# Kernel optimization log

Measured on AMD Instinct MI355X. Metric: run time of the kernel, lower is better.

Reference implementation:

```python
import jax, jax.numpy as jnp
import numpy as np

B, H, W, C = 8, 64, 64, 64
CFG = C // 8  # filters for f and g


def setup_inputs() -> dict:
    key = jax.random.key(0)
    kx, kf, kg, kh = jax.random.split(key, 4)
    x = jax.random.normal(kx, (B, H, W, C), dtype=jnp.float32)
    # 1x1 conv kernels, Keras layout (kh, kw, in_ch, out_ch); glorot-scale init
    kernel_f = jax.random.normal(kf, (1, 1, C, CFG), dtype=jnp.float32) * (2.0 / (C + CFG)) ** 0.5
    kernel_g = jax.random.normal(kg, (1, 1, C, CFG), dtype=jnp.float32) * (2.0 / (C + CFG)) ** 0.5
    kernel_h = jax.random.normal(kh, (1, 1, C, C), dtype=jnp.float32) * (2.0 / (C + C)) ** 0.5
    gamma = jnp.zeros((1,), dtype=jnp.float32)
    return {"x": x, "kernel_f": kernel_f, "kernel_g": kernel_g, "kernel_h": kernel_h, "gamma": gamma}


def reference(x, kernel_f, kernel_g, kernel_h, gamma):
    b, h, w, c = x.shape
    n = h * w
    xf = x.reshape(b, n, c)  # hw_flatten; 1x1 conv == per-pixel matmul
    f = jnp.einsum('bnc,cd->bnd', xf, kernel_f[0, 0])  # [B, N, C//8]
    g = jnp.einsum('bnc,cd->bnd', xf, kernel_g[0, 0])  # [B, N, C//8]
    hh = jnp.einsum('bnc,cd->bnd', xf, kernel_h[0, 0])  # [B, N, C]
    s = jnp.einsum('bqd,bkd->bqk', g, f)  # unscaled attention scores [B, N, N]
    beta = jax.nn.softmax(s, axis=-1)
    o = jnp.einsum('bqk,bkc->bqc', beta, hh).reshape(b, h, w, c)
    return gamma * o + x
```

## Files before the change

kernel.cpp:

```cpp
#include <hip/hip_runtime.h>
#include <hip/hip_bf16.h>


#define NPIX 4096
#define CH 64

typedef float f32x4 __attribute__((ext_vector_type(4)));
typedef short s16x8 __attribute__((ext_vector_type(8)));
typedef unsigned int u32x4 __attribute__((ext_vector_type(4)));
typedef unsigned short u16;
typedef unsigned int u32;
typedef unsigned long long u64;

__device__ __forceinline__ u16 f32_to_bf16(float f) {
  u32 u = __builtin_bit_cast(u32, f);
  u += 0x7fffu + ((u >> 16) & 1u);
  return (u16)(u >> 16);
}
__device__ __forceinline__ u32 pack_bf16(float lo, float hi) {
  return (u32)f32_to_bf16(lo) | ((u32)f32_to_bf16(hi) << 16);
}
__device__ __forceinline__ u32 cvt_pk_bf16(float lo, float hi) {
  u32 d;
  asm("v_cvt_pk_bf16_f32 %0, %1, %2" : "=v"(d) : "v"(lo), "v"(hi));
  return d;
}
__device__ __forceinline__ void gload_lds16(const void* g, void* l) {
  __builtin_amdgcn_global_load_lds(
      (const __attribute__((address_space(1))) unsigned int*)g,
      (__attribute__((address_space(3))) unsigned int*)l, 16, 0, 0);
}

__global__ __launch_bounds__(256, 2) void proj_kernel(
    const float* __restrict__ x, const float* __restrict__ kf,
    const float* __restrict__ kg, const float* __restrict__ kh,
    u16* __restrict__ Qg, u16* __restrict__ Kf, char* __restrict__ Vt) {
  __shared__ __align__(16) char Wt[80 * 128];
  __shared__ u16 fgs[16][68];

  const int t = threadIdx.x;
  const int b = blockIdx.x >> 6;
  const int chunk = blockIdx.x & 63;
  const int n0 = chunk << 6;

  for (int i = t; i < 4096; i += 256) {
    int cin = i >> 6, cout = i & 63;
    *(u16*)(Wt + cout * 128 + (((cin >> 3) ^ (cout & 7)) << 4) +
            ((cin & 7) << 1)) = f32_to_bf16(kh[i]);
  }
  for (int i = t; i < 512; i += 256) {
    int cin = i >> 3, d = i & 7;
    {
      int cout = 64 + d;
      *(u16*)(Wt + cout * 128 + (((cin >> 3) ^ (cout & 7)) << 4) +
              ((cin & 7) << 1)) = f32_to_bf16(kf[i]);
    }
    {
      int cout = 72 + d;
      *(u16*)(Wt + cout * 128 + (((cin >> 3) ^ (cout & 7)) << 4) +
              ((cin & 7) << 1)) = f32_to_bf16(kg[i] * 1.44269504088896f);
    }
  }

  const int w = t >> 6, l = t & 63;
  const int qr = l & 15, g = l >> 4;
  const int n = n0 + w * 16 + qr;

  s16x8 a[2];
  const float* xrow = x + ((size_t)b * NPIX + n) * CH;
#pragma unroll
  for (int ks = 0; ks < 2; ++ks) {
    f32x4 x0 = *(const f32x4*)(xrow + ks * 32 + g * 8);
    f32x4 x1 = *(const f32x4*)(xrow + ks * 32 + g * 8 + 4);
    u32x4 tmp = {pack_bf16(x0[0], x0[1]), pack_bf16(x0[2], x0[3]),
                 pack_bf16(x1[0], x1[1]), pack_bf16(x1[2], x1[3])};
    a[ks] = __builtin_bit_cast(s16x8, tmp);
  }
  __syncthreads();

  f32x4 acc[5];
#pragma unroll
  for (int nt = 0; nt < 5; ++nt) acc[nt] = (f32x4){0.f, 0.f, 0.f, 0.f};
#pragma unroll
  for (int ks = 0; ks < 2; ++ks) {
#pragma unroll
    for (int nt = 0; nt < 5; ++nt) {
      int cout = (nt < 4 ? nt * 16 : 64) + qr;
      int u = (ks << 2) + g;
      s16x8 bfr = *(const s16x8*)(Wt + cout * 128 + ((u ^ (cout & 7)) << 4));
      acc[nt] =
          __builtin_amdgcn_mfma_f32_16x16x32_bf16(a[ks], bfr, acc[nt], 0, 0, 0);
    }
  }

#pragma unroll
  for (int nt = 0; nt < 4; ++nt) {
    int c = nt * 16 + qr;
    u64 val = (u64)pack_bf16(acc[nt][0], acc[nt][1]) |
              ((u64)pack_bf16(acc[nt][2], acc[nt][3]) << 32);
    int t2v = ((chunk & 1) << 1) | (w >> 1);
    int p = (t2v << 2) | g;
    *(u64*)(Vt + (((size_t)(b * 64 + c) * 32 + (chunk >> 1)) << 8) +
            ((p ^ qr) << 4) + ((w & 1) << 3)) = val;
  }
#pragma unroll
  for (int r = 0; r < 4; ++r)
    fgs[qr][w * 16 + g * 4 + r] = f32_to_bf16(acc[4][r]);
  __syncthreads();
  if (t < 128) {
    int nn = t & 63;
    int rbase = (t < 64) ? 0 : 8;
    u16* dst = ((t < 64) ? Kf : Qg) + ((size_t)b * NPIX + n0 + nn) * 8;
    u32x4 o;
#pragma unroll
    for (int d = 0; d < 4; ++d)
      o[d] = (u32)fgs[rbase + 2 * d][nn] |
             ((u32)fgs[rbase + 2 * d + 1][nn] << 16);
    *(u32x4*)dst = o;
  }
}

__global__ __launch_bounds__(256, 4) void attn_kernel(
    const u16* __restrict__ Qg, const u16* __restrict__ Kf,
    const char* __restrict__ Vt, u16* __restrict__ Op, float* __restrict__ Lp,
    int logS) {
  __shared__ __align__(16) char Ks[2][2048];
  __shared__ __align__(16) char Vs[2][16384];

  const int t = threadIdx.x;
  const int b = blockIdx.x & 7;
  const int rest = blockIdx.x >> 3;
  const int smask = (1 << logS) - 1;
  const int ksplit = rest & smask;
  const int q0 = (rest >> logS) << 7;
  const int nch = 32 >> logS;
  const int w = t >> 6, l = t & 63;
  const int qr = l & 15, g = l >> 4;
  const int qw = q0 + w * 32;

  s16x8 qf0 = (s16x8){0, 0, 0, 0, 0, 0, 0, 0};
  s16x8 qf1 = (s16x8){0, 0, 0, 0, 0, 0, 0, 0};
  if (g == 0) {
    qf0 = *(const s16x8*)(Qg + ((size_t)b * NPIX + qw + qr) * 8);
    qf1 = *(const s16x8*)(Qg + ((size_t)b * NPIX + qw + 16 + qr) * 8);
  }

  const char* vbase = Vt + (size_t)b * (CH * NPIX * 2);
  const char* kbase = (const char*)Kf + (size_t)b * NPIX * 16;

  auto stage = [&](int buf, int kc) {
    if (w == 0) {
      gload_lds16(kbase + ((kc * 128 + l) << 4), &Ks[buf][0]);
      gload_lds16(kbase + ((kc * 128 + 64 + l) << 4), &Ks[buf][1024]);
    }
#pragma unroll
    for (int i = 0; i < 4; ++i) {
      int c = w * 16 + i * 4 + (l >> 4);
      gload_lds16(vbase + (((size_t)c * 32 + kc) << 8) + ((l & 15) << 4),
                  &Vs[buf][w * 4096 + i * 1024]);
    }
  };

  float lsum0 = 0.f, lsum1 = 0.f;
  f32x4 o0[4], o1[4];
#pragma unroll
  for (int fc = 0; fc < 4; ++fc) {
    o0[fc] = (f32x4){0.f, 0.f, 0.f, 0.f};
    o1[fc] = (f32x4){0.f, 0.f, 0.f, 0.f};
  }

  const int kc0 = ksplit * nch;
  stage(0, kc0);
  __syncthreads();

  s16x8 ak0 = (s16x8){0, 0, 0, 0, 0, 0, 0, 0};
  s16x8 ak1 = (s16x8){0, 0, 0, 0, 0, 0, 0, 0};

  for (int i = 0; i < nch; ++i) {
    const int buf = i & 1;
    if (i < nch - 1) stage(buf ^ 1, kc0 + i + 1);

    const f32x4 zz = (f32x4){0.f, 0.f, 0.f, 0.f};
#pragma unroll
    for (int t2 = 0; t2 < 4; ++t2) {
      if (g == 0) {
        ak0 = *(const s16x8*)&Ks[buf][(t2 * 32 + qr) * 16];
        ak1 = *(const s16x8*)&Ks[buf][(t2 * 32 + 16 + qr) * 16];
      }
      __builtin_amdgcn_s_setprio(1);
      f32x4 s00 = __builtin_amdgcn_mfma_f32_16x16x32_bf16(ak0, qf0, zz, 0, 0, 0);
      f32x4 s10 = __builtin_amdgcn_mfma_f32_16x16x32_bf16(ak0, qf1, zz, 0, 0, 0);
      f32x4 s01 = __builtin_amdgcn_mfma_f32_16x16x32_bf16(ak1, qf0, zz, 0, 0, 0);
      f32x4 s11 = __builtin_amdgcn_mfma_f32_16x16x32_bf16(ak1, qf1, zz, 0, 0, 0);
      __builtin_amdgcn_s_setprio(0);

      f32x4 e00, e01, e10, e11;
#pragma unroll
      for (int r = 0; r < 4; ++r) {
        e00[r] = __builtin_exp2f(s00[r]);
        e01[r] = __builtin_exp2f(s01[r]);
        e10[r] = __builtin_exp2f(s10[r]);
        e11[r] = __builtin_exp2f(s11[r]);
        lsum0 += e00[r] + e01[r];
        lsum1 += e10[r] + e11[r];
      }
      u32x4 aw0 = {cvt_pk_bf16(e00[0], e00[1]), cvt_pk_bf16(e00[2], e00[3]),
                   cvt_pk_bf16(e01[0], e01[1]), cvt_pk_bf16(e01[2], e01[3])};
      u32x4 aw1 = {cvt_pk_bf16(e10[0], e10[1]), cvt_pk_bf16(e10[2], e10[3]),
                   cvt_pk_bf16(e11[0], e11[1]), cvt_pk_bf16(e11[2], e11[3])};
      s16x8 af0 = __builtin_bit_cast(s16x8, aw0);
      s16x8 af1 = __builtin_bit_cast(s16x8, aw1);

      __builtin_amdgcn_s_setprio(1);
#pragma unroll
      for (int fc = 0; fc < 4; ++fc) {
        const s16x8 bv = *(const s16x8*)&Vs
            [buf][(fc * 16 + qr) * 256 + ((((t2 << 2) | g) ^ qr) << 4)];
        o0[fc] =
            __builtin_amdgcn_mfma_f32_16x16x32_bf16(af0, bv, o0[fc], 0, 0, 0);
        o1[fc] =
            __builtin_amdgcn_mfma_f32_16x16x32_bf16(af1, bv, o1[fc], 0, 0, 0);
      }
      __builtin_amdgcn_s_setprio(0);
    }
    __syncthreads();
  }

  lsum0 += __shfl_xor(lsum0, 16, 64);
  lsum0 += __shfl_xor(lsum0, 32, 64);
  lsum1 += __shfl_xor(lsum1, 16, 64);
  lsum1 += __shfl_xor(lsum1, 32, 64);
  const size_t rowbase = (size_t)ksplit * 32768 + (size_t)b * NPIX + qw;
  if (g == 0) {
    Lp[rowbase + qr] = lsum0;
    Lp[rowbase + 16 + qr] = lsum1;
  }
#pragma unroll
  for (int fc = 0; fc < 4; ++fc)
#pragma unroll
    for (int r = 0; r < 4; ++r) {
      Op[(rowbase + 4 * g + r) * 64 + fc * 16 + qr] = f32_to_bf16(o0[fc][r]);
      Op[(rowbase + 16 + 4 * g + r) * 64 + fc * 16 + qr] =
          f32_to_bf16(o1[fc][r]);
    }
}

__global__ __launch_bounds__(256, 4) void merge_kernel(
    const u16* __restrict__ Op, const float* __restrict__ Lp,
    const float* __restrict__ x, const float* __restrict__ gamma,
    float* __restrict__ out, int nsplit) {
  const int tid = blockIdx.x * 256 + threadIdx.x;
  const int r = tid >> 2;
  const int cg = (tid & 3) << 4;

  float wsum = 0.f;
  float acc[16];
#pragma unroll
  for (int i = 0; i < 16; ++i) acc[i] = 0.f;
  for (int s = 0; s < nsplit; ++s) {
    wsum += Lp[(size_t)s * 32768 + r];
    const u16* src = Op + ((size_t)s * 32768 + r) * 64 + cg;
    u32x4 a = *(const u32x4*)src;
    u32x4 b2 = *(const u32x4*)(src + 8);
#pragma unroll
    for (int j = 0; j < 4; ++j) {
      acc[2 * j] += __builtin_bit_cast(float, a[j] << 16);
      acc[2 * j + 1] += __builtin_bit_cast(float, a[j] & 0xffff0000u);
      acc[8 + 2 * j] += __builtin_bit_cast(float, b2[j] << 16);
      acc[8 + 2 * j + 1] += __builtin_bit_cast(float, b2[j] & 0xffff0000u);
    }
  }
  const float inv = 1.f / fmaxf(wsum, 1e-30f);
  const float gm = gamma[0];
  const size_t base = (size_t)r * 64 + cg;
#pragma unroll
  for (int j = 0; j < 4; ++j) {
    f32x4 xx = *(const f32x4*)(x + base + 4 * j);
    f32x4 o;
#pragma unroll
    for (int k2 = 0; k2 < 4; ++k2) {
      float val = acc[4 * j + k2] * inv;
      val = fminf(fmaxf(val, -1e30f), 1e30f);
      o[k2] = gm * val + xx[k2];
    }
    *(f32x4*)(out + base + 4 * j) = o;
  }
}

extern "C" void kernel_launch(void* const* d_in, const int* in_sizes, int n_in,
                              void* d_out, int out_size, void* d_ws,
                              size_t ws_size, hipStream_t stream) {
  const float* x = (const float*)d_in[0];
  const float* kf = (const float*)d_in[1];
  const float* kg = (const float*)d_in[2];
  const float* kh = (const float*)d_in[3];
  const float* gamma = (const float*)d_in[4];
  float* out = (float*)d_out;

  char* ws = (char*)d_ws;
  u16* Qg = (u16*)ws;
  u16* Kf = (u16*)(ws + (512u << 10));
  char* Vt = ws + (1u << 20);
  u16* Op = (u16*)(ws + (5u << 20));

  int logS;
  if (ws_size >= (23u << 20)) logS = 2;
  else if (ws_size >= (14u << 20)) logS = 1;
  else logS = 0;
  const int SPLIT = 1 << logS;
  float* Lp = (float*)(ws + (5u << 20) + (size_t)SPLIT * (4u << 20));

  hipLaunchKernelGGL(proj_kernel, dim3(512), dim3(256), 0, stream, x, kf, kg,
                     kh, Qg, Kf, Vt);
  hipLaunchKernelGGL(attn_kernel, dim3(256 * SPLIT), dim3(256), 0, stream, Qg,
                     Kf, Vt, Op, Lp, logS);
  hipLaunchKernelGGL(merge_kernel, dim3(512), dim3(256), 0, stream, Op, Lp, x,
                     gamma, out, SPLIT);
}
```

Measured before the change: 129.4 us.

## Single-buffer V tile to raise occupancy and allow 8-way key split

Drops the double buffer for the V tile in LDS, halving shared memory per block, and raises the launch bound to 8 blocks per CU. V loads for the next chunk now happen after compute, behind an extra barrier, so they no longer overlap with MFMA work. A larger workspace also enables an 8-way key split (logS=3), which gives more blocks at the cost of more partial outputs to merge. The aim is to hide latency through occupancy instead of software pipelining, though each chunk now waits on its V load.

```diff
diff --git a/kernel.cpp b/kernel.cpp
--- a/kernel.cpp
+++ b/kernel.cpp
@@ -120,12 +120,12 @@
   }
 }
 
-__global__ __launch_bounds__(256, 4) void attn_kernel(
+__global__ __launch_bounds__(256, 8) void attn_kernel(
     const u16* __restrict__ Qg, const u16* __restrict__ Kf,
     const char* __restrict__ Vt, u16* __restrict__ Op, float* __restrict__ Lp,
     int logS) {
   __shared__ __align__(16) char Ks[2][2048];
-  __shared__ __align__(16) char Vs[2][16384];
+  __shared__ __align__(16) char Vs[16384];
 
   const int t = threadIdx.x;
   const int b = blockIdx.x & 7;
@@ -148,16 +148,18 @@
   const char* vbase = Vt + (size_t)b * (CH * NPIX * 2);
   const char* kbase = (const char*)Kf + (size_t)b * NPIX * 16;
 
-  auto stage = [&](int buf, int kc) {
+  auto stage_K = [&](int kb, int kc) {
     if (w == 0) {
-      gload_lds16(kbase + ((kc * 128 + l) << 4), &Ks[buf][0]);
-      gload_lds16(kbase + ((kc * 128 + 64 + l) << 4), &Ks[buf][1024]);
-    }
-#pragma unroll
-    for (int i = 0; i < 4; ++i) {
-      int c = w * 16 + i * 4 + (l >> 4);
+      gload_lds16(kbase + ((kc * 128 + l) << 4), &Ks[kb][0]);
+      gload_lds16(kbase + ((kc * 128 + 64 + l) << 4), &Ks[kb][1024]);
+    }
+  };
+  auto stage_V = [&](int kc) {
+#pragma unroll
+    for (int i2 = 0; i2 < 4; ++i2) {
+      int c = w * 16 + i2 * 4 + (l >> 4);
       gload_lds16(vbase + (((size_t)c * 32 + kc) << 8) + ((l & 15) << 4),
-                  &Vs[buf][w * 4096 + i * 1024]);
+                  &Vs[w * 4096 + i2 * 1024]);
     }
   };
 
@@ -170,22 +172,23 @@
   }
 
   const int kc0 = ksplit * nch;
-  stage(0, kc0);
+  stage_K(0, kc0);
+  stage_V(kc0);
   __syncthreads();
 
   s16x8 ak0 = (s16x8){0, 0, 0, 0, 0, 0, 0, 0};
   s16x8 ak1 = (s16x8){0, 0, 0, 0, 0, 0, 0, 0};
 
   for (int i = 0; i < nch; ++i) {
-    const int buf = i & 1;
-    if (i < nch - 1) stage(buf ^ 1, kc0 + i + 1);
+    const int kb = i & 1;
+    if (i < nch - 1) stage_K(kb ^ 1, kc0 + i + 1);
 
     const f32x4 zz = (f32x4){0.f, 0.f, 0.f, 0.f};
 #pragma unroll
     for (int t2 = 0; t2 < 4; ++t2) {
       if (g == 0) {
-        ak0 = *(const s16x8*)&Ks[buf][(t2 * 32 + qr) * 16];
-        ak1 = *(const s16x8*)&Ks[buf][(t2 * 32 + 16 + qr) * 16];
+        ak0 = *(const s16x8*)&Ks[kb][(t2 * 32 + qr) * 16];
+        ak1 = *(const s16x8*)&Ks[kb][(t2 * 32 + 16 + qr) * 16];
       }
       __builtin_amdgcn_s_setprio(1);
       f32x4 s00 = __builtin_amdgcn_mfma_f32_16x16x32_bf16(ak0, qf0, zz, 0, 0, 0);
@@ -215,7 +218,7 @@
 #pragma unroll
       for (int fc = 0; fc < 4; ++fc) {
         const s16x8 bv = *(const s16x8*)&Vs
-            [buf][(fc * 16 + qr) * 256 + ((((t2 << 2) | g) ^ qr) << 4)];
+            [(fc * 16 + qr) * 256 + ((((t2 << 2) | g) ^ qr) << 4)];
         o0[fc] =
             __builtin_amdgcn_mfma_f32_16x16x32_bf16(af0, bv, o0[fc], 0, 0, 0);
         o1[fc] =
@@ -223,7 +226,12 @@
       }
       __builtin_amdgcn_s_setprio(0);
     }
+
     __syncthreads();
+    if (i < nch - 1) {
+      stage_V(kc0 + i + 1);
+      __syncthreads();
+    }
   }
 
   lsum0 += __shfl_xor(lsum0, 16, 64);
@@ -304,7 +312,8 @@
   u16* Op = (u16*)(ws + (5u << 20));
 
   int logS;
-  if (ws_size >= (23u << 20)) logS = 2;
+  if (ws_size >= (39u << 20)) logS = 3;
+  else if (ws_size >= (23u << 20)) logS = 2;
   else if (ws_size >= (14u << 20)) logS = 1;
   else logS = 0;
   const int SPLIT = 1 << logS;
```

New measurement: 516.4 us. 3.99x slower.
